# Kernel optimization log

Hardware: AMD Instinct MI355X
Metric: run time of the kernel (lower is better)

The kernel has to match this reference:

```python
import jax, jax.numpy as jnp
import numpy as np

N_WIRES = 4
N_LAYERS = 2
PATCHES = 196  # 14x14 grid of 2x2 patches


def _bexp(a, nd):
    # broadcast angle to rank nd by appending singleton axes
    a = jnp.asarray(a)
    return a.reshape(a.shape + (1,) * (nd - a.ndim))


def _apply_ry(state, wire, angle):
    # state: [B, P, 2,2,2,2]; angle broadcastable to [B, P] or scalar
    st = jnp.moveaxis(state, 2 + wire, -1)
    c = _bexp(jnp.cos(angle * 0.5), st.ndim - 1)
    s = _bexp(jnp.sin(angle * 0.5), st.ndim - 1)
    s0, s1 = st[..., 0], st[..., 1]
    out = jnp.stack([c * s0 - s * s1, s * s0 + c * s1], axis=-1)
    return jnp.moveaxis(out, -1, 2 + wire)


def _apply_cnot(state, control, target):
    st = jnp.moveaxis(state, (2 + control, 2 + target), (-2, -1))
    st = jnp.stack([st[..., 0, :], st[..., 1, ::-1]], axis=-2)
    return jnp.moveaxis(st, (-2, -1), (2 + control, 2 + target))


def _measure_z(state):
    # PauliZ expectation on each wire: sum probs * (+1/-1)
    p = state * state  # real state => |amp|^2
    outs = []
    for w in range(N_WIRES):
        axes = tuple(a for a in range(2, 2 + N_WIRES) if a != 2 + w)
        m = p.sum(axis=axes)  # [B, P, 2]
        outs.append(m[..., 0] - m[..., 1])
    return jnp.stack(outs, axis=-1)  # [B, P, 4]


def _quanv(x, theta):
    B = x.shape[0]
    # extract 2x2 patches: order (r,c),(r,c+1),(r+1,c),(r+1,c+1)
    img = x.reshape(B, 14, 2, 14, 2).transpose(0, 1, 3, 2, 4).reshape(B, PATCHES, 4)
    state = jnp.zeros((B, PATCHES, 16), x.dtype).at[:, :, 0].set(1.0)
    state = state.reshape(B, PATCHES, 2, 2, 2, 2)
    # encoder: RY(x_i) on wire i
    for w in range(N_WIRES):
        state = _apply_ry(state, w, img[:, :, w])
    # variational layers: trainable RY per wire + CNOT ring
    for l in range(N_LAYERS):
        for w in range(N_WIRES):
            state = _apply_ry(state, w, theta[l, w])
        for w in range(N_WIRES):
            state = _apply_cnot(state, w, (w + 1) % N_WIRES)
    return _measure_z(state).reshape(B, PATCHES * N_WIRES)  # [B, 784]


def setup_inputs() -> dict:
    key = jax.random.key(0)
    k = jax.random.split(key, 6)
    B = 4096
    return {
        "x": jax.random.uniform(k[0], (B, 784), jnp.float32),
        "theta": jax.random.normal(k[1], (N_LAYERS, N_WIRES), jnp.float32),
        "W1": jax.random.normal(k[2], (784, 128), jnp.float32) * 0.05,
        "b1": jnp.zeros((128,), jnp.float32),
        "W2": jax.random.normal(k[3], (128, 10), jnp.float32) * 0.05,
        "b2": jnp.zeros((10,), jnp.float32),
    }


def reference(x, theta, W1, b1, W2, b2):
    feats = _quanv(x, theta)                 # [B, 784]
    h = jax.nn.relu(feats @ W1 + b1)          # [B, 128]
    logits = h @ W2 + b2                      # [B, 10]
    return jax.nn.log_softmax(logits, axis=-1)
```

## Files before the change

kernel.cpp:

```cpp
#include <hip/hip_runtime.h>
#include <math.h>

#define PATCHES 196
#define KPAD 800
#define MROWS 8
#define CIRC (MROWS * PATCHES)
#define THREADS 512
#define FRAG_ELEMS (25 * 64 * 8)

typedef short short8 __attribute__((ext_vector_type(8)));
typedef float f32x4 __attribute__((ext_vector_type(4)));

__device__ __forceinline__ unsigned short f2bf(float f) {
  union { float f; unsigned u; } x; x.f = f;
  unsigned r = x.u + 0x7fff + ((x.u >> 16) & 1);
  return (unsigned short)(r >> 16);
}

__global__ __launch_bounds__(256) void w1t_pack_kernel(
    const float* __restrict__ W1, unsigned short* __restrict__ w1p) {
  int idx = blockIdx.x * 256 + threadIdx.x;
  if (idx >= 128 * KPAD) return;
  int n = idx / KPAD;
  int k = idx - n * KPAD;
  float v = (k < 784) ? W1[k * 128 + n] : 0.f;
  int ki = k >> 5;
  int quad = (k & 31) >> 3;
  int j = k & 7;
  w1p[(n >> 4) * FRAG_ELEMS + (ki * 64 + quad * 16 + (n & 15)) * 8 + j] = f2bf(v);
}

__device__ __forceinline__ void apply_ry(float st[16], int bit, float c, float s) {
#pragma unroll
  for (int i = 0; i < 16; ++i) {
    if (!(i & bit)) {
      int j = i | bit;
      float a0 = st[i], a1 = st[j];
      st[i] = c * a0 - s * a1;
      st[j] = s * a0 + c * a1;
    }
  }
}

__device__ __forceinline__ void apply_cnot(float st[16], int cb, int tb) {
#pragma unroll
  for (int i = 0; i < 16; ++i) {
    if ((i & cb) && !(i & tb)) {
      int j = i | tb;
      float t = st[i]; st[i] = st[j]; st[j] = t;
    }
  }
}

__global__ __launch_bounds__(THREADS) void fused_kernel(
    const float* __restrict__ x, const float* __restrict__ theta,
    const unsigned short* __restrict__ w1p, const float* __restrict__ b1,
    const float* __restrict__ W2, const float* __restrict__ b2,
    float* __restrict__ out) {
  __shared__ unsigned short afr[FRAG_ELEMS];
  __shared__ float ws2[1280];
  __shared__ float hs[MROWS * 132];
  __shared__ float ls[MROWS * 10];

  const int tid = threadIdx.x;
  const int row0 = blockIdx.x * MROWS;

  {
    ushort4 z; z.x = z.y = z.z = z.w = 0;
    for (int s = tid; s < FRAG_ELEMS / 4; s += THREADS)
      reinterpret_cast<ushort4*>(afr)[s] = z;
  }
  if (tid < 320)
    reinterpret_cast<float4*>(ws2)[tid] = reinterpret_cast<const float4*>(W2)[tid];

  float tc[8], ts[8];
#pragma unroll
  for (int w = 0; w < 8; ++w) {
    float a = 0.5f * theta[w];
    tc[w] = __cosf(a);
    ts[w] = __sinf(a);
  }

  const int nit = (CIRC - tid + THREADS - 1) / THREADS;
  float2 xcA, xcB;
  {
    int bl = tid / PATCHES;
    int p = tid - bl * PATCHES;
    int pr = p / 14, pc = p - pr * 14;
    const float* xp = x + (size_t)(row0 + bl) * 784 + pr * 56 + pc * 2;
    xcA = *reinterpret_cast<const float2*>(xp);
    xcB = *reinterpret_cast<const float2*>(xp + 28);
  }
  __syncthreads();

#pragma unroll 1
  for (int i = 0; i < nit; ++i) {
    const int c = tid + i * THREADS;
    float2 xnA = xcA, xnB = xcB;
    if (i + 1 < nit) {
      const int cn = c + THREADS;
      int bl = cn / PATCHES;
      int p = cn - bl * PATCHES;
      int pr = p / 14, pc = p - pr * 14;
      const float* xp = x + (size_t)(row0 + bl) * 784 + pr * 56 + pc * 2;
      xnA = *reinterpret_cast<const float2*>(xp);
      xnB = *reinterpret_cast<const float2*>(xp + 28);
    }

    float c0 = __cosf(0.5f * xcA.x), s0 = __sinf(0.5f * xcA.x);
    float c1 = __cosf(0.5f * xcA.y), s1 = __sinf(0.5f * xcA.y);
    float c2 = __cosf(0.5f * xcB.x), s2 = __sinf(0.5f * xcB.x);
    float c3 = __cosf(0.5f * xcB.y), s3 = __sinf(0.5f * xcB.y);
    float u00 = c0 * c1, u01 = c0 * s1, u10 = s0 * c1, u11 = s0 * s1;
    float w00 = c2 * c3, w01 = c2 * s3, w10 = s2 * c3, w11 = s2 * s3;

    float st[16];
    st[ 0] = u00 * w00; st[ 1] = u00 * w01; st[ 2] = u00 * w10; st[ 3] = u00 * w11;
    st[ 4] = u01 * w00; st[ 5] = u01 * w01; st[ 6] = u01 * w10; st[ 7] = u01 * w11;
    st[ 8] = u10 * w00; st[ 9] = u10 * w01; st[10] = u10 * w10; st[11] = u10 * w11;
    st[12] = u11 * w00; st[13] = u11 * w01; st[14] = u11 * w10; st[15] = u11 * w11;

#pragma unroll
    for (int l = 0; l < 2; ++l) {
      apply_ry(st, 8, tc[l * 4 + 0], ts[l * 4 + 0]);
      apply_ry(st, 4, tc[l * 4 + 1], ts[l * 4 + 1]);
      apply_ry(st, 2, tc[l * 4 + 2], ts[l * 4 + 2]);
      apply_ry(st, 1, tc[l * 4 + 3], ts[l * 4 + 3]);
      apply_cnot(st, 8, 4);
      apply_cnot(st, 4, 2);
      apply_cnot(st, 2, 1);
      apply_cnot(st, 1, 8);
    }

    float m0 = 0.f, m1 = 0.f, m2 = 0.f, m3 = 0.f;
#pragma unroll
    for (int q = 0; q < 16; ++q) {
      float p2 = st[q] * st[q];
      m0 += (q & 8) ? -p2 : p2;
      m1 += (q & 4) ? -p2 : p2;
      m2 += (q & 2) ? -p2 : p2;
      m3 += (q & 1) ? -p2 : p2;
    }

    {
      int bl = c / PATCHES;
      int p = c - bl * PATCHES;
      int K = p * 4;
      int ki = K >> 5;
      int quad = (K & 31) >> 3;
      int j0 = K & 7;
      ushort4 o;
      o.x = f2bf(m0); o.y = f2bf(m1); o.z = f2bf(m2); o.w = f2bf(m3);
      *reinterpret_cast<ushort4*>(afr + (ki * 64 + quad * 16 + bl) * 8 + j0) = o;
    }

    xcA = xnA; xcB = xnB;
  }
  __syncthreads();

  const int lane = tid & 63;
  const int wave = tid >> 6;
  const int m = lane & 15;
  const int quad = lane >> 4;

  {
    const unsigned short* bp = w1p + (size_t)wave * FRAG_ELEMS + lane * 8;
    const unsigned short* apl = afr + lane * 8;

    f32x4 acc = {0.f, 0.f, 0.f, 0.f};

#pragma unroll 1
    for (int kc = 0; kc < 5; ++kc) {
      short8 a[5], b[5];
#pragma unroll
      for (int u = 0; u < 5; ++u) {
        const int ki = kc * 5 + u;
        a[u] = *reinterpret_cast<const short8*>(apl + ki * 512);
        b[u] = *reinterpret_cast<const short8*>(bp + ki * 512);
      }
#pragma unroll
      for (int u = 0; u < 5; ++u)
        acc = __builtin_amdgcn_mfma_f32_16x16x32_bf16(a[u], b[u], acc, 0, 0, 0);
    }

    if (quad < 2) {
      const int col = wave * 16 + m;
      const float bc = b1[col];
#pragma unroll
      for (int r = 0; r < 4; ++r)
        hs[(quad * 4 + r) * 132 + col] = fmaxf(acc[r] + bc, 0.f);
    }
  }
  __syncthreads();

  if (tid < MROWS * 10) {
    const int r = tid / 10;
    const int k = tid - r * 10;
    float a = b2[k];
    const float* hr = hs + r * 132;
#pragma unroll 8
    for (int jj = 0; jj < 128; ++jj) a = fmaf(hr[jj], ws2[jj * 10 + k], a);
    ls[tid] = a;
  }
  __syncthreads();

  if (tid < MROWS) {
    const int r = tid;
    float mx = ls[r * 10];
#pragma unroll
    for (int k = 1; k < 10; ++k) mx = fmaxf(mx, ls[r * 10 + k]);
    float sum = 0.f;
#pragma unroll
    for (int k = 0; k < 10; ++k) sum += __expf(ls[r * 10 + k] - mx);
    const float lse = mx + __logf(sum);
    float* orow = out + (size_t)(row0 + r) * 10;
#pragma unroll
    for (int k = 0; k < 10; ++k) orow[k] = ls[r * 10 + k] - lse;
  }
}

extern "C" void kernel_launch(void* const* d_in, const int* in_sizes, int n_in,
                              void* d_out, int out_size, void* d_ws, size_t ws_size,
                              hipStream_t stream) {
  const float* x     = (const float*)d_in[0];
  const float* theta = (const float*)d_in[1];
  const float* W1    = (const float*)d_in[2];
  const float* b1    = (const float*)d_in[3];
  const float* W2    = (const float*)d_in[4];
  const float* b2    = (const float*)d_in[5];
  float* out = (float*)d_out;

  const int B = in_sizes[0] / 784;

  unsigned short* w1p = (unsigned short*)d_ws;

  w1t_pack_kernel<<<(128 * KPAD + 255) / 256, 256, 0, stream>>>(W1, w1p);
  fused_kernel<<<B / MROWS, THREADS, 0, stream>>>(x, theta, w1p, b1, W2, b2, out);
}
```

Baseline: 83.98 us.

## Vectorize quantum circuit with float2 pairs and prefetch W1 fragments early

```diff
diff --git a/kernel.cpp b/kernel.cpp
--- a/kernel.cpp
+++ b/kernel.cpp
@@ -10,6 +10,7 @@
 
 typedef short short8 __attribute__((ext_vector_type(8)));
 typedef float f32x4 __attribute__((ext_vector_type(4)));
+typedef float f2 __attribute__((ext_vector_type(2)));
 
 __device__ __forceinline__ unsigned short f2bf(float f) {
   union { float f; unsigned u; } x; x.f = f;
@@ -30,26 +31,16 @@
   w1p[(n >> 4) * FRAG_ELEMS + (ki * 64 + quad * 16 + (n & 15)) * 8 + j] = f2bf(v);
 }
 
-__device__ __forceinline__ void apply_ry(float st[16], int bit, float c, float s) {
-#pragma unroll
-  for (int i = 0; i < 16; ++i) {
-    if (!(i & bit)) {
-      int j = i | bit;
-      float a0 = st[i], a1 = st[j];
-      st[i] = c * a0 - s * a1;
-      st[j] = s * a0 + c * a1;
-    }
-  }
-}
-
-__device__ __forceinline__ void apply_cnot(float st[16], int cb, int tb) {
-#pragma unroll
-  for (int i = 0; i < 16; ++i) {
-    if ((i & cb) && !(i & tb)) {
-      int j = i | tb;
-      float t = st[i]; st[i] = st[j]; st[j] = t;
-    }
-  }
+
+__device__ __forceinline__ void ry_pair(f2& lo, f2& hi, float c, float s) {
+  f2 a = lo, b = hi;
+  lo = c * a - s * b;
+  hi = s * a + c * b;
+}
+__device__ __forceinline__ f2 ry_in(f2 v, float c, float s) {
+  f2 sw = v.yx;
+  f2 ms = {-s, s};
+  return c * v + ms * sw;
 }
 
 __global__ __launch_bounds__(THREADS) void fused_kernel(
@@ -63,7 +54,15 @@
   __shared__ float ls[MROWS * 10];
 
   const int tid = threadIdx.x;
+  const int lane = tid & 63;
+  const int wave = tid >> 6;
   const int row0 = blockIdx.x * MROWS;
+
+  const unsigned short* bp = w1p + (size_t)wave * FRAG_ELEMS + lane * 8;
+  short8 bpf[8];
+#pragma unroll
+  for (int u = 0; u < 8; ++u)
+    bpf[u] = *reinterpret_cast<const short8*>(bp + u * 512);
 
   {
     ushort4 z; z.x = z.y = z.z = z.w = 0;
@@ -73,38 +72,38 @@
   if (tid < 320)
     reinterpret_cast<float4*>(ws2)[tid] = reinterpret_cast<const float4*>(W2)[tid];
 
-  float tc[8], ts[8];
+  float tc[8], tsn[8];
 #pragma unroll
   for (int w = 0; w < 8; ++w) {
     float a = 0.5f * theta[w];
     tc[w] = __cosf(a);
-    ts[w] = __sinf(a);
+    tsn[w] = __sinf(a);
   }
 
   const int nit = (CIRC - tid + THREADS - 1) / THREADS;
-  float2 xcA, xcB;
+  f2 xcA, xcB;
   {
     int bl = tid / PATCHES;
     int p = tid - bl * PATCHES;
     int pr = p / 14, pc = p - pr * 14;
     const float* xp = x + (size_t)(row0 + bl) * 784 + pr * 56 + pc * 2;
-    xcA = *reinterpret_cast<const float2*>(xp);
-    xcB = *reinterpret_cast<const float2*>(xp + 28);
+    xcA = *reinterpret_cast<const f2*>(xp);
+    xcB = *reinterpret_cast<const f2*>(xp + 28);
   }
   __syncthreads();
 
 #pragma unroll 1
   for (int i = 0; i < nit; ++i) {
     const int c = tid + i * THREADS;
-    float2 xnA = xcA, xnB = xcB;
+    f2 xnA = xcA, xnB = xcB;
     if (i + 1 < nit) {
       const int cn = c + THREADS;
       int bl = cn / PATCHES;
       int p = cn - bl * PATCHES;
       int pr = p / 14, pc = p - pr * 14;
       const float* xp = x + (size_t)(row0 + bl) * 784 + pr * 56 + pc * 2;
-      xnA = *reinterpret_cast<const float2*>(xp);
-      xnB = *reinterpret_cast<const float2*>(xp + 28);
+      xnA = *reinterpret_cast<const f2*>(xp);
+      xnB = *reinterpret_cast<const f2*>(xp + 28);
     }
 
     float c0 = __cosf(0.5f * xcA.x), s0 = __sinf(0.5f * xcA.x);
@@ -112,35 +111,59 @@
     float c2 = __cosf(0.5f * xcB.x), s2 = __sinf(0.5f * xcB.x);
     float c3 = __cosf(0.5f * xcB.y), s3 = __sinf(0.5f * xcB.y);
     float u00 = c0 * c1, u01 = c0 * s1, u10 = s0 * c1, u11 = s0 * s1;
-    float w00 = c2 * c3, w01 = c2 * s3, w10 = s2 * c3, w11 = s2 * s3;
-
-    float st[16];
-    st[ 0] = u00 * w00; st[ 1] = u00 * w01; st[ 2] = u00 * w10; st[ 3] = u00 * w11;
-    st[ 4] = u01 * w00; st[ 5] = u01 * w01; st[ 6] = u01 * w10; st[ 7] = u01 * w11;
-    st[ 8] = u10 * w00; st[ 9] = u10 * w01; st[10] = u10 * w10; st[11] = u10 * w11;
-    st[12] = u11 * w00; st[13] = u11 * w01; st[14] = u11 * w10; st[15] = u11 * w11;
+    f2 wlo = {c2 * c3, c2 * s3};
+    f2 whi = {s2 * c3, s2 * s3};
+
+    f2 st2[8];
+    st2[0] = u00 * wlo; st2[1] = u00 * whi;
+    st2[2] = u01 * wlo; st2[3] = u01 * whi;
+    st2[4] = u10 * wlo; st2[5] = u10 * whi;
+    st2[6] = u11 * wlo; st2[7] = u11 * whi;
 
 #pragma unroll
     for (int l = 0; l < 2; ++l) {
-      apply_ry(st, 8, tc[l * 4 + 0], ts[l * 4 + 0]);
-      apply_ry(st, 4, tc[l * 4 + 1], ts[l * 4 + 1]);
-      apply_ry(st, 2, tc[l * 4 + 2], ts[l * 4 + 2]);
-      apply_ry(st, 1, tc[l * 4 + 3], ts[l * 4 + 3]);
-      apply_cnot(st, 8, 4);
-      apply_cnot(st, 4, 2);
-      apply_cnot(st, 2, 1);
-      apply_cnot(st, 1, 8);
-    }
-
-    float m0 = 0.f, m1 = 0.f, m2 = 0.f, m3 = 0.f;
-#pragma unroll
-    for (int q = 0; q < 16; ++q) {
-      float p2 = st[q] * st[q];
-      m0 += (q & 8) ? -p2 : p2;
-      m1 += (q & 4) ? -p2 : p2;
-      m2 += (q & 2) ? -p2 : p2;
-      m3 += (q & 1) ? -p2 : p2;
-    }
+      const int b = l * 4;
+      ry_pair(st2[0], st2[4], tc[b + 0], tsn[b + 0]);
+      ry_pair(st2[1], st2[5], tc[b + 0], tsn[b + 0]);
+      ry_pair(st2[2], st2[6], tc[b + 0], tsn[b + 0]);
+      ry_pair(st2[3], st2[7], tc[b + 0], tsn[b + 0]);
+      ry_pair(st2[0], st2[2], tc[b + 1], tsn[b + 1]);
+      ry_pair(st2[1], st2[3], tc[b + 1], tsn[b + 1]);
+      ry_pair(st2[4], st2[6], tc[b + 1], tsn[b + 1]);
+      ry_pair(st2[5], st2[7], tc[b + 1], tsn[b + 1]);
+      ry_pair(st2[0], st2[1], tc[b + 2], tsn[b + 2]);
+      ry_pair(st2[2], st2[3], tc[b + 2], tsn[b + 2]);
+      ry_pair(st2[4], st2[5], tc[b + 2], tsn[b + 2]);
+      ry_pair(st2[6], st2[7], tc[b + 2], tsn[b + 2]);
+#pragma unroll
+      for (int k = 0; k < 8; ++k) st2[k] = ry_in(st2[k], tc[b + 3], tsn[b + 3]);
+      { f2 t = st2[4]; st2[4] = st2[6]; st2[6] = t; }
+      { f2 t = st2[5]; st2[5] = st2[7]; st2[7] = t; }
+      { f2 t = st2[2]; st2[2] = st2[3]; st2[3] = t; }
+      { f2 t = st2[6]; st2[6] = st2[7]; st2[7] = t; }
+      st2[1] = st2[1].yx; st2[3] = st2[3].yx;
+      st2[5] = st2[5].yx; st2[7] = st2[7].yx;
+#pragma unroll
+      for (int k = 0; k < 4; ++k) {
+        f2 a = st2[k], bb = st2[k + 4];
+        st2[k]     = (f2){a.x, bb.y};
+        st2[k + 4] = (f2){bb.x, a.y};
+      }
+    }
+
+    float h[8], d[8];
+#pragma unroll
+    for (int k = 0; k < 8; ++k) {
+      f2 p2 = st2[k] * st2[k];
+      h[k] = p2.x + p2.y;
+      d[k] = p2.x - p2.y;
+    }
+    float a0 = h[0] + h[1], a1 = h[2] + h[3], a2 = h[4] + h[5], a3 = h[6] + h[7];
+    float b0 = h[0] - h[1], b1 = h[2] - h[3], b2 = h[4] - h[5], b3 = h[6] - h[7];
+    float m0 = (a0 + a1) - (a2 + a3);
+    float m1 = (a0 - a1) + (a2 - a3);
+    float m2 = (b0 + b1) + (b2 + b3);
+    float m3 = ((d[0] + d[1]) + (d[2] + d[3])) + ((d[4] + d[5]) + (d[6] + d[7]));
 
     {
       int bl = c / PATCHES;
@@ -158,29 +181,19 @@
   }
   __syncthreads();
 
-  const int lane = tid & 63;
-  const int wave = tid >> 6;
   const int m = lane & 15;
   const int quad = lane >> 4;
 
   {
-    const unsigned short* bp = w1p + (size_t)wave * FRAG_ELEMS + lane * 8;
     const unsigned short* apl = afr + lane * 8;
-
     f32x4 acc = {0.f, 0.f, 0.f, 0.f};
 
-#pragma unroll 1
-    for (int kc = 0; kc < 5; ++kc) {
-      short8 a[5], b[5];
-#pragma unroll
-      for (int u = 0; u < 5; ++u) {
-        const int ki = kc * 5 + u;
-        a[u] = *reinterpret_cast<const short8*>(apl + ki * 512);
-        b[u] = *reinterpret_cast<const short8*>(bp + ki * 512);
-      }
-#pragma unroll
-      for (int u = 0; u < 5; ++u)
-        acc = __builtin_amdgcn_mfma_f32_16x16x32_bf16(a[u], b[u], acc, 0, 0, 0);
+#pragma unroll
+    for (int ki = 0; ki < 25; ++ki) {
+      short8 a = *reinterpret_cast<const short8*>(apl + ki * 512);
+      short8 b = (ki < 8) ? bpf[ki]
+                          : *reinterpret_cast<const short8*>(bp + ki * 512);
+      acc = __builtin_amdgcn_mfma_f32_16x16x32_bf16(a, b, acc, 0, 0, 0);
     }
 
     if (quad < 2) {
```

New measurement: 83.14 us. No clear change (-1.0%).
